# Optimization experiments

Hardware: AMD Instinct MI355X
Metric: run time of the kernel (lower is better)

Reference implementation:

```python
import jax, jax.numpy as jnp
import numpy as np


def setup_inputs() -> dict:
    key = jax.random.key(0)
    k1, k2, k3 = jax.random.split(key, 3)
    B, M, N, D = 8, 12, 32, 256
    C = N * N          # Conv2d channel dim == N*N (see permute/view in source)
    R = 2              # reduction
    x = jax.random.normal(k1, (B, M, N, D), dtype=jnp.float32)
    W1 = jax.random.normal(k2, (C // R, C), dtype=jnp.float32) * 0.02  # Conv2d(C, C//R, 1, bias=False)
    W2 = jax.random.normal(k3, (C, C // R), dtype=jnp.float32) * 0.02  # Conv2d(C//R, C, 1, bias=False)
    return {"x": x, "W1": W1, "W2": W2}


def _mycorr(x):
    # Pearson correlation across feature dim D -> [B, M, N, N] adjacency
    xm = x - x.mean(axis=-1, keepdims=True)
    cov = jnp.einsum('bmnd,bmkd->bmnk', xm, xm)
    diag = jnp.diagonal(cov, axis1=-2, axis2=-1)                 # [B, M, N]
    norm = jnp.sqrt(jnp.clip(diag, 1e-12))
    return cov / (norm[..., :, None] * norm[..., None, :])


def reference(x, W1, W2):
    B, M, N, D = x.shape
    adj = _mycorr(x)

    # Fused pairwise-combo + mean over concat dim (2D):
    #   cat([Wh_i, pos_ij * Wh_j], -1).mean(-1) = (sum_d Wh_i + sum_d pos_ij*Wh_j) / (2D)
    # pos_ij[d] = 1 where Wh_i[d] == Wh_j[d] else 2   (source's where(diff==0, 1, 2))
    Wi = x[:, :, :, None, :]          # [B, M, N, 1, D]
    Wj = x[:, :, None, :, :]          # [B, M, 1, N, D]
    pos = jnp.where(Wi == Wj, jnp.float32(1.0), jnp.float32(2.0))
    e0 = (x.sum(-1)[:, :, :, None] + (pos * Wj).sum(-1)) / (2.0 * D)  # [B, M, N, N]

    # squeeze-excite style 1x1-conv MLP over the N*N channel dim
    ef = e0.reshape(B, M, N * N).transpose(0, 2, 1)                   # [B, C=N*N, M]
    h = jax.nn.relu(jnp.einsum('oc,bcm->bom', W1, ef))                # [B, C//R, M]
    e2 = jnp.einsum('co,bom->bcm', W2, h)                             # [B, C, M]
    e = jax.nn.sigmoid(e2.transpose(0, 2, 1).reshape(B, M, N, N))

    att = jnp.where(adj > 0, e, jnp.float32(-1e12))
    att = jax.nn.softmax(att, axis=-1)
    return jnp.einsum('bmnk,bmkd->bmnd', att, x)
```

## Files before the change

kernel.cpp:

```cpp
#include <hip/hip_runtime.h>


__device__ __forceinline__ float dot4(float4 a, float4 b) {
    return a.x*b.x + a.y*b.y + a.z*b.z + a.w*b.w;
}
__device__ __forceinline__ void fma4(float4& acc, float s, float4 v) {
    acc.x += s*v.x; acc.y += s*v.y; acc.z += s*v.z; acc.w += s*v.w;
}

__global__ __launch_bounds__(256) void kS(const float* __restrict__ x,
                                          float* __restrict__ Ssum) {
    int bm = blockIdx.x;
    const float4* x4 = (const float4*)x;
    int n = threadIdx.x >> 3, dq = threadIdx.x & 7;
    float s = 0.f;
    #pragma unroll
    for (int j = 0; j < 8; ++j) {
        float4 v = x4[bm*2048 + n*64 + dq + 8*j];
        s += v.x + v.y + v.z + v.w;
    }
    s += __shfl_xor(s, 1, 8);
    s += __shfl_xor(s, 2, 8);
    s += __shfl_xor(s, 4, 8);
    if (dq == 0) Ssum[bm*32 + n] = s;
}

__global__ __launch_bounds__(256) void k2(const float* __restrict__ W1,
                                          const float* __restrict__ Ssum,
                                          float* __restrict__ Ht) {
    __shared__ float S_l[8][32];
    __shared__ float ef[8][1024];
    int t = threadIdx.x;
    int clane = t & 15, og = t >> 4;
    int oT = blockIdx.x, bmG = blockIdx.y;
    {
        int bl = t >> 5, n = t & 31;
        S_l[bl][n] = Ssum[(bmG*8 + bl)*32 + n];
    }
    __syncthreads();
    #pragma unroll
    for (int i = 0; i < 32; ++i) {
        int idx = t + 256*i;
        int bl = idx >> 10, c = idx & 1023;
        int nn = c >> 5, kk = c & 31;
        float sn = S_l[bl][nn], sk = S_l[bl][kk];
        ef[bl][c] = (sn + 2.f*sk - (nn == kk ? sk : 0.f)) * (1.f/512.f);
    }
    __syncthreads();
    int o = oT*16 + og;
    const float4* w4 = (const float4*)(W1 + o*1024);
    float acc[8] = {0.f,0.f,0.f,0.f,0.f,0.f,0.f,0.f};
    #pragma unroll
    for (int co = 0; co < 16; ++co) {
        float4 w = w4[co*16 + clane];
        #pragma unroll
        for (int bl = 0; bl < 8; ++bl) {
            float4 e = *((const float4*)&ef[bl][(co*16 + clane)*4]);
            acc[bl] += dot4(w, e);
        }
    }
    #pragma unroll
    for (int bl = 0; bl < 8; ++bl) {
        float a = acc[bl];
        a += __shfl_xor(a, 1, 16);
        a += __shfl_xor(a, 2, 16);
        a += __shfl_xor(a, 4, 16);
        a += __shfl_xor(a, 8, 16);
        acc[bl] = a;
    }
    if (clane == 0) {
        #pragma unroll
        for (int bl = 0; bl < 8; ++bl)
            Ht[(bmG*8 + bl)*512 + o] = fmaxf(acc[bl], 0.f);
    }
}

__global__ __launch_bounds__(256) void k3(const float* __restrict__ W2,
                                          const float* __restrict__ Ht,
                                          float* __restrict__ Et) {
    __shared__ float hl[8][512];
    int t = threadIdx.x;
    int olane = t & 15, cg = t >> 4;
    int cT = blockIdx.x, bmG = blockIdx.y;
    const float4* Ht4 = (const float4*)Ht;
    #pragma unroll
    for (int i = 0; i < 4; ++i) {
        int idx = t + 256*i;
        int bl = idx >> 7, o4 = idx & 127;
        *((float4*)&hl[bl][o4*4]) = Ht4[(bmG*8 + bl)*128 + o4];
    }
    __syncthreads();
    int c = cT*16 + cg;
    const float4* w4 = (const float4*)(W2 + c*512);
    float acc[8] = {0.f,0.f,0.f,0.f,0.f,0.f,0.f,0.f};
    #pragma unroll
    for (int oo = 0; oo < 8; ++oo) {
        float4 w = w4[oo*16 + olane];
        #pragma unroll
        for (int bl = 0; bl < 8; ++bl) {
            float4 h = *((const float4*)&hl[bl][(oo*16 + olane)*4]);
            acc[bl] += dot4(w, h);
        }
    }
    #pragma unroll
    for (int bl = 0; bl < 8; ++bl) {
        float a = acc[bl];
        a += __shfl_xor(a, 1, 16);
        a += __shfl_xor(a, 2, 16);
        a += __shfl_xor(a, 4, 16);
        a += __shfl_xor(a, 8, 16);
        acc[bl] = a;
    }
    if (olane == 0) {
        #pragma unroll
        for (int bl = 0; bl < 8; ++bl)
            Et[(bmG*8 + bl)*1024 + c] = 1.f / (1.f + __expf(-acc[bl]));
    }
}

__global__ __launch_bounds__(256) void k4(const float* __restrict__ x,
                                          const float* __restrict__ Ssum,
                                          const float* __restrict__ Et,
                                          float* __restrict__ out) {
    int bm = blockIdx.x >> 1;
    int h  = blockIdx.x & 1;
    int t  = threadIdx.x;
    __shared__ float4 xs4[32][65];
    __shared__ float att_l[32][36];
    __shared__ float S_l[32];

    const float4* x4 = (const float4*)x;
    #pragma unroll
    for (int i = 0; i < 8; ++i) {
        int idx = t + 256*i;
        xs4[idx >> 6][idx & 63] = x4[bm*2048 + idx];
    }
    if (t < 32) S_l[t] = Ssum[bm*32 + t];
    __syncthreads();

    {
        int a = t >> 4, b = t & 15;
        float g00=0.f, g01=0.f, g10=0.f, g11=0.f;
        #pragma unroll 8
        for (int q = 0; q < 64; ++q) {
            float4 a0 = xs4[a][q],    a1 = xs4[a+16][q];
            float4 b0 = xs4[b][q],    b1 = xs4[b+16][q];
            g00 += dot4(a0,b0); g01 += dot4(a0,b1);
            g10 += dot4(a1,b0); g11 += dot4(a1,b1);
        }
        float sa0 = S_l[a]    * (1.f/256.f);
        float sa1 = S_l[a+16] * (1.f/256.f);
        float sb0 = S_l[b], sb1 = S_l[b+16];
        float e00 = Et[bm*1024 + a*32 + b];
        float e01 = Et[bm*1024 + a*32 + b+16];
        float e10 = Et[bm*1024 + (a+16)*32 + b];
        float e11 = Et[bm*1024 + (a+16)*32 + b+16];
        att_l[a][b]       = (g00 - sa0*sb0) > 0.f ? e00 : -1e12f;
        att_l[a][b+16]    = (g01 - sa0*sb1) > 0.f ? e01 : -1e12f;
        att_l[a+16][b]    = (g10 - sa1*sb0) > 0.f ? e10 : -1e12f;
        att_l[a+16][b+16] = (g11 - sa1*sb1) > 0.f ? e11 : -1e12f;
    }
    __syncthreads();

    {
        int r = t >> 3, q = t & 7;
        float4 lg = *((const float4*)&att_l[r][q*4]);
        float m = fmaxf(fmaxf(lg.x,lg.y), fmaxf(lg.z,lg.w));
        m = fmaxf(m, __shfl_xor(m,1,8));
        m = fmaxf(m, __shfl_xor(m,2,8));
        m = fmaxf(m, __shfl_xor(m,4,8));
        float4 p;
        p.x = __expf(lg.x-m); p.y = __expf(lg.y-m);
        p.z = __expf(lg.z-m); p.w = __expf(lg.w-m);
        float s = p.x+p.y+p.z+p.w;
        s += __shfl_xor(s,1,8);
        s += __shfl_xor(s,2,8);
        s += __shfl_xor(s,4,8);
        float inv = 1.f/s;
        p.x*=inv; p.y*=inv; p.z*=inv; p.w*=inv;
        *((float4*)&att_l[r][q*4]) = p;
    }
    __syncthreads();

    {
        int txl = t & 31, wy = t >> 5;
        int r0 = wy*4;
        float4 acc0={0,0,0,0}, acc1={0,0,0,0}, acc2={0,0,0,0}, acc3={0,0,0,0};
        #pragma unroll
        for (int kq = 0; kq < 8; ++kq) {
            float4 xa = xs4[kq*4+0][h*32 + txl];
            float4 xb = xs4[kq*4+1][h*32 + txl];
            float4 xc = xs4[kq*4+2][h*32 + txl];
            float4 xd = xs4[kq*4+3][h*32 + txl];
            float4 w0 = *((const float4*)&att_l[r0+0][kq*4]);
            float4 w1 = *((const float4*)&att_l[r0+1][kq*4]);
            float4 w2 = *((const float4*)&att_l[r0+2][kq*4]);
            float4 w3 = *((const float4*)&att_l[r0+3][kq*4]);
            fma4(acc0,w0.x,xa); fma4(acc0,w0.y,xb); fma4(acc0,w0.z,xc); fma4(acc0,w0.w,xd);
            fma4(acc1,w1.x,xa); fma4(acc1,w1.y,xb); fma4(acc1,w1.z,xc); fma4(acc1,w1.w,xd);
            fma4(acc2,w2.x,xa); fma4(acc2,w2.y,xb); fma4(acc2,w2.z,xc); fma4(acc2,w2.w,xd);
            fma4(acc3,w3.x,xa); fma4(acc3,w3.y,xb); fma4(acc3,w3.z,xc); fma4(acc3,w3.w,xd);
        }
        float4* out4 = (float4*)out;
        out4[bm*2048 + (r0+0)*64 + h*32 + txl] = acc0;
        out4[bm*2048 + (r0+1)*64 + h*32 + txl] = acc1;
        out4[bm*2048 + (r0+2)*64 + h*32 + txl] = acc2;
        out4[bm*2048 + (r0+3)*64 + h*32 + txl] = acc3;
    }
}

extern "C" void kernel_launch(void* const* d_in, const int* in_sizes, int n_in,
                              void* d_out, int out_size, void* d_ws, size_t ws_size,
                              hipStream_t stream) {
    const float* x  = (const float*)d_in[0];
    const float* W1 = (const float*)d_in[1];
    const float* W2 = (const float*)d_in[2];
    float* out = (float*)d_out;
    float* ws  = (float*)d_ws;

    float* Ssum = ws;
    float* Ht   = ws + 3072;
    float* Et   = ws + 52224;

    kS<<<96, 256, 0, stream>>>(x, Ssum);
    k2<<<dim3(32, 12), 256, 0, stream>>>(W1, Ssum, Ht);
    k3<<<dim3(64, 12), 256, 0, stream>>>(W2, Ht, Et);
    k4<<<192, 256, 0, stream>>>(x, Ssum, Et, out);
}
```

Baseline: 81.55 us.

## Fuse four kernels into one cooperative kernel with grid syncs

Replaces the four launches (row sums, first MLP layer, second MLP layer, attention) with a single cooperative kernel of 192 blocks that separates the phases with grid.sync and reuses one shared-memory union across them. Each block now computes more MLP outputs (2 and 4 rows per thread), and the row sums are recomputed per block instead of stored in a buffer. The aim is to remove launch gaps between the small kernels. In exchange the MLP phases run on fewer blocks and pay for grid-wide barriers.

```diff
diff --git a/kernel.cpp b/kernel.cpp
--- a/kernel.cpp
+++ b/kernel.cpp
@@ -1,4 +1,7 @@
 #include <hip/hip_runtime.h>
+#include <hip/hip_cooperative_groups.h>
+
+namespace cg = cooperative_groups;
 
 
 __device__ __forceinline__ float dot4(float4 a, float4 b) {
@@ -8,204 +11,248 @@
     acc.x += s*v.x; acc.y += s*v.y; acc.z += s*v.z; acc.w += s*v.w;
 }
 
-__global__ __launch_bounds__(256) void kS(const float* __restrict__ x,
-                                          float* __restrict__ Ssum) {
-    int bm = blockIdx.x;
+union SMem {
+    struct { float S[8][32]; float ef[8][1024]; } p1;
+    struct { float hl[8][512]; } p2;
+    struct { float4 xs4[32][65]; float att[32][36]; float S[32]; } p3;
+};
+
+__global__ __launch_bounds__(256) void fused(
+        const float* __restrict__ x, const float* __restrict__ W1,
+        const float* __restrict__ W2, float* __restrict__ out,
+        float* __restrict__ Ht, float* __restrict__ Et)
+{
+    cg::grid_group grid = cg::this_grid();
+    __shared__ SMem sm;
+    const int t = threadIdx.x;
+    const int bid = blockIdx.x;
     const float4* x4 = (const float4*)x;
-    int n = threadIdx.x >> 3, dq = threadIdx.x & 7;
-    float s = 0.f;
-    #pragma unroll
-    for (int j = 0; j < 8; ++j) {
-        float4 v = x4[bm*2048 + n*64 + dq + 8*j];
-        s += v.x + v.y + v.z + v.w;
+
+    {
+        const int bmG = bid >> 4, oT = bid & 15;
+        {
+            const int n = t >> 3, dq = t & 7;
+            #pragma unroll
+            for (int bl = 0; bl < 8; ++bl) {
+                const float4* xb = x4 + (bmG*8 + bl)*2048;
+                float s = 0.f;
+                #pragma unroll
+                for (int j = 0; j < 8; ++j) {
+                    float4 v = xb[n*64 + dq + 8*j];
+                    s += v.x + v.y + v.z + v.w;
+                }
+                s += __shfl_xor(s, 1, 8);
+                s += __shfl_xor(s, 2, 8);
+                s += __shfl_xor(s, 4, 8);
+                if (dq == 0) sm.p1.S[bl][n] = s;
+            }
+        }
+        __syncthreads();
+        #pragma unroll
+        for (int i = 0; i < 32; ++i) {
+            int idx = t + 256*i;
+            int bl = idx >> 10, c = idx & 1023;
+            int nn = c >> 5, kk = c & 31;
+            float sn = sm.p1.S[bl][nn], sk = sm.p1.S[bl][kk];
+            sm.p1.ef[bl][c] = (sn + 2.f*sk - (nn == kk ? sk : 0.f)) * (1.f/512.f);
+        }
+        __syncthreads();
+        const int clane = t & 15, og = t >> 4;
+        const int o0 = oT*32 + og;
+        const float4* w40 = (const float4*)(W1 + o0*1024);
+        const float4* w41 = (const float4*)(W1 + (o0+16)*1024);
+        float acc0[8] = {0.f,0.f,0.f,0.f,0.f,0.f,0.f,0.f};
+        float acc1[8] = {0.f,0.f,0.f,0.f,0.f,0.f,0.f,0.f};
+        #pragma unroll
+        for (int co = 0; co < 16; ++co) {
+            float4 e[8];
+            #pragma unroll
+            for (int bl = 0; bl < 8; ++bl)
+                e[bl] = *((const float4*)&sm.p1.ef[bl][(co*16 + clane)*4]);
+            float4 wa = w40[co*16 + clane];
+            float4 wb = w41[co*16 + clane];
+            #pragma unroll
+            for (int bl = 0; bl < 8; ++bl) {
+                acc0[bl] += dot4(wa, e[bl]);
+                acc1[bl] += dot4(wb, e[bl]);
+            }
+        }
+        #pragma unroll
+        for (int bl = 0; bl < 8; ++bl) {
+            float a = acc0[bl], b = acc1[bl];
+            a += __shfl_xor(a, 1, 16); b += __shfl_xor(b, 1, 16);
+            a += __shfl_xor(a, 2, 16); b += __shfl_xor(b, 2, 16);
+            a += __shfl_xor(a, 4, 16); b += __shfl_xor(b, 4, 16);
+            a += __shfl_xor(a, 8, 16); b += __shfl_xor(b, 8, 16);
+            acc0[bl] = a; acc1[bl] = b;
+        }
+        if (clane == 0) {
+            #pragma unroll
+            for (int bl = 0; bl < 8; ++bl) {
+                int row = (bmG*8 + bl)*512;
+                Ht[row + o0]      = fmaxf(acc0[bl], 0.f);
+                Ht[row + o0 + 16] = fmaxf(acc1[bl], 0.f);
+            }
+        }
     }
-    s += __shfl_xor(s, 1, 8);
-    s += __shfl_xor(s, 2, 8);
-    s += __shfl_xor(s, 4, 8);
-    if (dq == 0) Ssum[bm*32 + n] = s;
-}
-
-__global__ __launch_bounds__(256) void k2(const float* __restrict__ W1,
-                                          const float* __restrict__ Ssum,
-                                          float* __restrict__ Ht) {
-    __shared__ float S_l[8][32];
-    __shared__ float ef[8][1024];
-    int t = threadIdx.x;
-    int clane = t & 15, og = t >> 4;
-    int oT = blockIdx.x, bmG = blockIdx.y;
+    __threadfence();
+    grid.sync();
+
     {
-        int bl = t >> 5, n = t & 31;
-        S_l[bl][n] = Ssum[(bmG*8 + bl)*32 + n];
+        const int bmG = bid >> 4, cQ = bid & 15;
+        const float4* Ht4 = (const float4*)Ht;
+        #pragma unroll
+        for (int i = 0; i < 4; ++i) {
+            int idx = t + 256*i;
+            int bl = idx >> 7, o4 = idx & 127;
+            *((float4*)&sm.p2.hl[bl][o4*4]) = Ht4[(bmG*8 + bl)*128 + o4];
+        }
+        __syncthreads();
+        const int olane = t & 15, cgp = t >> 4;
+        const int c0 = cQ*64 + cgp;
+        const float4* w4a = (const float4*)(W2 + (c0     )*512);
+        const float4* w4b = (const float4*)(W2 + (c0 + 16)*512);
+        const float4* w4c = (const float4*)(W2 + (c0 + 32)*512);
+        const float4* w4d = (const float4*)(W2 + (c0 + 48)*512);
+        float accA[8] = {0.f,0.f,0.f,0.f,0.f,0.f,0.f,0.f};
+        float accB[8] = {0.f,0.f,0.f,0.f,0.f,0.f,0.f,0.f};
+        float accC[8] = {0.f,0.f,0.f,0.f,0.f,0.f,0.f,0.f};
+        float accD[8] = {0.f,0.f,0.f,0.f,0.f,0.f,0.f,0.f};
+        #pragma unroll
+        for (int oo = 0; oo < 8; ++oo) {
+            float4 hv[8];
+            #pragma unroll
+            for (int bl = 0; bl < 8; ++bl)
+                hv[bl] = *((const float4*)&sm.p2.hl[bl][(oo*16 + olane)*4]);
+            float4 wa = w4a[oo*16 + olane];
+            float4 wb = w4b[oo*16 + olane];
+            float4 wc = w4c[oo*16 + olane];
+            float4 wd = w4d[oo*16 + olane];
+            #pragma unroll
+            for (int bl = 0; bl < 8; ++bl) {
+                accA[bl] += dot4(wa, hv[bl]);
+                accB[bl] += dot4(wb, hv[bl]);
+                accC[bl] += dot4(wc, hv[bl]);
+                accD[bl] += dot4(wd, hv[bl]);
+            }
+        }
+        #pragma unroll
+        for (int bl = 0; bl < 8; ++bl) {
+            float a = accA[bl], b = accB[bl], c = accC[bl], d = accD[bl];
+            #pragma unroll
+            for (int m = 1; m < 16; m <<= 1) {
+                a += __shfl_xor(a, m, 16);
+                b += __shfl_xor(b, m, 16);
+                c += __shfl_xor(c, m, 16);
+                d += __shfl_xor(d, m, 16);
+            }
+            accA[bl]=a; accB[bl]=b; accC[bl]=c; accD[bl]=d;
+        }
+        if (olane == 0) {
+            #pragma unroll
+            for (int bl = 0; bl < 8; ++bl) {
+                int row = (bmG*8 + bl)*1024;
+                Et[row + c0]      = 1.f/(1.f + __expf(-accA[bl]));
+                Et[row + c0 + 16] = 1.f/(1.f + __expf(-accB[bl]));
+                Et[row + c0 + 32] = 1.f/(1.f + __expf(-accC[bl]));
+                Et[row + c0 + 48] = 1.f/(1.f + __expf(-accD[bl]));
+            }
+        }
     }
-    __syncthreads();
-    #pragma unroll
-    for (int i = 0; i < 32; ++i) {
-        int idx = t + 256*i;
-        int bl = idx >> 10, c = idx & 1023;
-        int nn = c >> 5, kk = c & 31;
-        float sn = S_l[bl][nn], sk = S_l[bl][kk];
-        ef[bl][c] = (sn + 2.f*sk - (nn == kk ? sk : 0.f)) * (1.f/512.f);
-    }
-    __syncthreads();
-    int o = oT*16 + og;
-    const float4* w4 = (const float4*)(W1 + o*1024);
-    float acc[8] = {0.f,0.f,0.f,0.f,0.f,0.f,0.f,0.f};
-    #pragma unroll
-    for (int co = 0; co < 16; ++co) {
-        float4 w = w4[co*16 + clane];
-        #pragma unroll
-        for (int bl = 0; bl < 8; ++bl) {
-            float4 e = *((const float4*)&ef[bl][(co*16 + clane)*4]);
-            acc[bl] += dot4(w, e);
-        }
-    }
-    #pragma unroll
-    for (int bl = 0; bl < 8; ++bl) {
-        float a = acc[bl];
-        a += __shfl_xor(a, 1, 16);
-        a += __shfl_xor(a, 2, 16);
-        a += __shfl_xor(a, 4, 16);
-        a += __shfl_xor(a, 8, 16);
-        acc[bl] = a;
-    }
-    if (clane == 0) {
-        #pragma unroll
-        for (int bl = 0; bl < 8; ++bl)
-            Ht[(bmG*8 + bl)*512 + o] = fmaxf(acc[bl], 0.f);
-    }
-}
-
-__global__ __launch_bounds__(256) void k3(const float* __restrict__ W2,
-                                          const float* __restrict__ Ht,
-                                          float* __restrict__ Et) {
-    __shared__ float hl[8][512];
-    int t = threadIdx.x;
-    int olane = t & 15, cg = t >> 4;
-    int cT = blockIdx.x, bmG = blockIdx.y;
-    const float4* Ht4 = (const float4*)Ht;
-    #pragma unroll
-    for (int i = 0; i < 4; ++i) {
-        int idx = t + 256*i;
-        int bl = idx >> 7, o4 = idx & 127;
-        *((float4*)&hl[bl][o4*4]) = Ht4[(bmG*8 + bl)*128 + o4];
-    }
-    __syncthreads();
-    int c = cT*16 + cg;
-    const float4* w4 = (const float4*)(W2 + c*512);
-    float acc[8] = {0.f,0.f,0.f,0.f,0.f,0.f,0.f,0.f};
-    #pragma unroll
-    for (int oo = 0; oo < 8; ++oo) {
-        float4 w = w4[oo*16 + olane];
-        #pragma unroll
-        for (int bl = 0; bl < 8; ++bl) {
-            float4 h = *((const float4*)&hl[bl][(oo*16 + olane)*4]);
-            acc[bl] += dot4(w, h);
-        }
-    }
-    #pragma unroll
-    for (int bl = 0; bl < 8; ++bl) {
-        float a = acc[bl];
-        a += __shfl_xor(a, 1, 16);
-        a += __shfl_xor(a, 2, 16);
-        a += __shfl_xor(a, 4, 16);
-        a += __shfl_xor(a, 8, 16);
-        acc[bl] = a;
-    }
-    if (olane == 0) {
-        #pragma unroll
-        for (int bl = 0; bl < 8; ++bl)
-            Et[(bmG*8 + bl)*1024 + c] = 1.f / (1.f + __expf(-acc[bl]));
-    }
-}
-
-__global__ __launch_bounds__(256) void k4(const float* __restrict__ x,
-                                          const float* __restrict__ Ssum,
-                                          const float* __restrict__ Et,
-                                          float* __restrict__ out) {
-    int bm = blockIdx.x >> 1;
-    int h  = blockIdx.x & 1;
-    int t  = threadIdx.x;
-    __shared__ float4 xs4[32][65];
-    __shared__ float att_l[32][36];
-    __shared__ float S_l[32];
-
-    const float4* x4 = (const float4*)x;
-    #pragma unroll
-    for (int i = 0; i < 8; ++i) {
-        int idx = t + 256*i;
-        xs4[idx >> 6][idx & 63] = x4[bm*2048 + idx];
-    }
-    if (t < 32) S_l[t] = Ssum[bm*32 + t];
-    __syncthreads();
+    __threadfence();
+    grid.sync();
 
     {
-        int a = t >> 4, b = t & 15;
-        float g00=0.f, g01=0.f, g10=0.f, g11=0.f;
-        #pragma unroll 8
-        for (int q = 0; q < 64; ++q) {
-            float4 a0 = xs4[a][q],    a1 = xs4[a+16][q];
-            float4 b0 = xs4[b][q],    b1 = xs4[b+16][q];
-            g00 += dot4(a0,b0); g01 += dot4(a0,b1);
-            g10 += dot4(a1,b0); g11 += dot4(a1,b1);
-        }
-        float sa0 = S_l[a]    * (1.f/256.f);
-        float sa1 = S_l[a+16] * (1.f/256.f);
-        float sb0 = S_l[b], sb1 = S_l[b+16];
-        float e00 = Et[bm*1024 + a*32 + b];
-        float e01 = Et[bm*1024 + a*32 + b+16];
-        float e10 = Et[bm*1024 + (a+16)*32 + b];
-        float e11 = Et[bm*1024 + (a+16)*32 + b+16];
-        att_l[a][b]       = (g00 - sa0*sb0) > 0.f ? e00 : -1e12f;
-        att_l[a][b+16]    = (g01 - sa0*sb1) > 0.f ? e01 : -1e12f;
-        att_l[a+16][b]    = (g10 - sa1*sb0) > 0.f ? e10 : -1e12f;
-        att_l[a+16][b+16] = (g11 - sa1*sb1) > 0.f ? e11 : -1e12f;
-    }
-    __syncthreads();
-
-    {
-        int r = t >> 3, q = t & 7;
-        float4 lg = *((const float4*)&att_l[r][q*4]);
-        float m = fmaxf(fmaxf(lg.x,lg.y), fmaxf(lg.z,lg.w));
-        m = fmaxf(m, __shfl_xor(m,1,8));
-        m = fmaxf(m, __shfl_xor(m,2,8));
-        m = fmaxf(m, __shfl_xor(m,4,8));
-        float4 p;
-        p.x = __expf(lg.x-m); p.y = __expf(lg.y-m);
-        p.z = __expf(lg.z-m); p.w = __expf(lg.w-m);
-        float s = p.x+p.y+p.z+p.w;
-        s += __shfl_xor(s,1,8);
-        s += __shfl_xor(s,2,8);
-        s += __shfl_xor(s,4,8);
-        float inv = 1.f/s;
-        p.x*=inv; p.y*=inv; p.z*=inv; p.w*=inv;
-        *((float4*)&att_l[r][q*4]) = p;
-    }
-    __syncthreads();
-
-    {
-        int txl = t & 31, wy = t >> 5;
-        int r0 = wy*4;
-        float4 acc0={0,0,0,0}, acc1={0,0,0,0}, acc2={0,0,0,0}, acc3={0,0,0,0};
-        #pragma unroll
-        for (int kq = 0; kq < 8; ++kq) {
-            float4 xa = xs4[kq*4+0][h*32 + txl];
-            float4 xb = xs4[kq*4+1][h*32 + txl];
-            float4 xc = xs4[kq*4+2][h*32 + txl];
-            float4 xd = xs4[kq*4+3][h*32 + txl];
-            float4 w0 = *((const float4*)&att_l[r0+0][kq*4]);
-            float4 w1 = *((const float4*)&att_l[r0+1][kq*4]);
-            float4 w2 = *((const float4*)&att_l[r0+2][kq*4]);
-            float4 w3 = *((const float4*)&att_l[r0+3][kq*4]);
-            fma4(acc0,w0.x,xa); fma4(acc0,w0.y,xb); fma4(acc0,w0.z,xc); fma4(acc0,w0.w,xd);
-            fma4(acc1,w1.x,xa); fma4(acc1,w1.y,xb); fma4(acc1,w1.z,xc); fma4(acc1,w1.w,xd);
-            fma4(acc2,w2.x,xa); fma4(acc2,w2.y,xb); fma4(acc2,w2.z,xc); fma4(acc2,w2.w,xd);
-            fma4(acc3,w3.x,xa); fma4(acc3,w3.y,xb); fma4(acc3,w3.z,xc); fma4(acc3,w3.w,xd);
-        }
-        float4* out4 = (float4*)out;
-        out4[bm*2048 + (r0+0)*64 + h*32 + txl] = acc0;
-        out4[bm*2048 + (r0+1)*64 + h*32 + txl] = acc1;
-        out4[bm*2048 + (r0+2)*64 + h*32 + txl] = acc2;
-        out4[bm*2048 + (r0+3)*64 + h*32 + txl] = acc3;
+        const int bm = bid >> 1, hh = bid & 1;
+        #pragma unroll
+        for (int i = 0; i < 8; ++i) {
+            int idx = t + 256*i;
+            sm.p3.xs4[idx >> 6][idx & 63] = x4[bm*2048 + idx];
+        }
+        __syncthreads();
+        {
+            int r = t >> 3, dq = t & 7;
+            float s = 0.f;
+            #pragma unroll
+            for (int j = 0; j < 8; ++j) {
+                float4 v = sm.p3.xs4[r][dq + 8*j];
+                s += v.x + v.y + v.z + v.w;
+            }
+            s += __shfl_xor(s, 1, 8);
+            s += __shfl_xor(s, 2, 8);
+            s += __shfl_xor(s, 4, 8);
+            if (dq == 0) sm.p3.S[r] = s;
+        }
+        __syncthreads();
+        {
+            int a = t >> 4, b = t & 15;
+            float g00=0.f, g01=0.f, g10=0.f, g11=0.f;
+            #pragma unroll 8
+            for (int q = 0; q < 64; ++q) {
+                float4 a0 = sm.p3.xs4[a][q],    a1 = sm.p3.xs4[a+16][q];
+                float4 b0 = sm.p3.xs4[b][q],    b1 = sm.p3.xs4[b+16][q];
+                g00 += dot4(a0,b0); g01 += dot4(a0,b1);
+                g10 += dot4(a1,b0); g11 += dot4(a1,b1);
+            }
+            float sa0 = sm.p3.S[a]    * (1.f/256.f);
+            float sa1 = sm.p3.S[a+16] * (1.f/256.f);
+            float sb0 = sm.p3.S[b], sb1 = sm.p3.S[b+16];
+            const float* Eb = Et + bm*1024;
+            float e00 = Eb[a*32 + b];
+            float e01 = Eb[a*32 + b+16];
+            float e10 = Eb[(a+16)*32 + b];
+            float e11 = Eb[(a+16)*32 + b+16];
+            sm.p3.att[a][b]       = (g00 - sa0*sb0) > 0.f ? e00 : -1e12f;
+            sm.p3.att[a][b+16]    = (g01 - sa0*sb1) > 0.f ? e01 : -1e12f;
+            sm.p3.att[a+16][b]    = (g10 - sa1*sb0) > 0.f ? e10 : -1e12f;
+            sm.p3.att[a+16][b+16] = (g11 - sa1*sb1) > 0.f ? e11 : -1e12f;
+        }
+        __syncthreads();
+        {
+            int r = t >> 3, q = t & 7;
+            float4 lg = *((const float4*)&sm.p3.att[r][q*4]);
+            float m = fmaxf(fmaxf(lg.x,lg.y), fmaxf(lg.z,lg.w));
+            m = fmaxf(m, __shfl_xor(m,1,8));
+            m = fmaxf(m, __shfl_xor(m,2,8));
+            m = fmaxf(m, __shfl_xor(m,4,8));
+            float4 p;
+            p.x = __expf(lg.x-m); p.y = __expf(lg.y-m);
+            p.z = __expf(lg.z-m); p.w = __expf(lg.w-m);
+            float s = p.x+p.y+p.z+p.w;
+            s += __shfl_xor(s,1,8);
+            s += __shfl_xor(s,2,8);
+            s += __shfl_xor(s,4,8);
+            float inv = 1.f/s;
+            p.x*=inv; p.y*=inv; p.z*=inv; p.w*=inv;
+            *((float4*)&sm.p3.att[r][q*4]) = p;
+        }
+        __syncthreads();
+        {
+            int txl = t & 31, wy = t >> 5;
+            int r0 = wy*4;
+            float4 acc0={0,0,0,0}, acc1={0,0,0,0}, acc2={0,0,0,0}, acc3={0,0,0,0};
+            #pragma unroll
+            for (int kq = 0; kq < 8; ++kq) {
+                float4 xa = sm.p3.xs4[kq*4+0][hh*32 + txl];
+                float4 xb = sm.p3.xs4[kq*4+1][hh*32 + txl];
+                float4 xc = sm.p3.xs4[kq*4+2][hh*32 + txl];
+                float4 xd = sm.p3.xs4[kq*4+3][hh*32 + txl];
+                float4 w0 = *((const float4*)&sm.p3.att[r0+0][kq*4]);
+                float4 w1 = *((const float4*)&sm.p3.att[r0+1][kq*4]);
+                float4 w2 = *((const float4*)&sm.p3.att[r0+2][kq*4]);
+                float4 w3 = *((const float4*)&sm.p3.att[r0+3][kq*4]);
+                fma4(acc0,w0.x,xa); fma4(acc0,w0.y,xb); fma4(acc0,w0.z,xc); fma4(acc0,w0.w,xd);
+                fma4(acc1,w1.x,xa); fma4(acc1,w1.y,xb); fma4(acc1,w1.z,xc); fma4(acc1,w1.w,xd);
+                fma4(acc2,w2.x,xa); fma4(acc2,w2.y,xb); fma4(acc2,w2.z,xc); fma4(acc2,w2.w,xd);
+                fma4(acc3,w3.x,xa); fma4(acc3,w3.y,xb); fma4(acc3,w3.z,xc); fma4(acc3,w3.w,xd);
+            }
+            float4* out4 = (float4*)out;
+            int base = bm*2048 + hh*32 + txl;
+            out4[base + (r0+0)*64] = acc0;
+            out4[base + (r0+1)*64] = acc1;
+            out4[base + (r0+2)*64] = acc2;
+            out4[base + (r0+3)*64] = acc3;
+        }
     }
 }
 
@@ -218,12 +265,11 @@
     float* out = (float*)d_out;
     float* ws  = (float*)d_ws;
 
-    float* Ssum = ws;
-    float* Ht   = ws + 3072;
-    float* Et   = ws + 52224;
-
-    kS<<<96, 256, 0, stream>>>(x, Ssum);
-    k2<<<dim3(32, 12), 256, 0, stream>>>(W1, Ssum, Ht);
-    k3<<<dim3(64, 12), 256, 0, stream>>>(W2, Ht, Et);
-    k4<<<192, 256, 0, stream>>>(x, Ssum, Et, out);
-}
+    float* Ht = ws;
+    float* Et = ws + 49152;
+
+    void* args[] = { (void*)&x, (void*)&W1, (void*)&W2,
+                     (void*)&out, (void*)&Ht, (void*)&Et };
+    hipLaunchCooperativeKernel((const void*)fused, dim3(192), dim3(256),
+                               args, 0, stream);
+}
```

New measurement: 173.7 us. 2.13x slower.
